# Performance work log

Measured on AMD Instinct MI355X. Metric: run time of the kernel, lower is better.

Reference implementation:

```python
import jax, jax.numpy as jnp
import numpy as np

NUM_HEADS = 16
SRC_FACTS = 4


def setup_inputs() -> dict:
    key = jax.random.key(0)
    k1, k2, k3, k4, k5 = jax.random.split(key, 5)
    B, S, H, Dh = 16, 512, NUM_HEADS, 64  # B = batch(4) * src_facts(4)
    D = H * Dh  # d_model = 1024
    pre_q = jax.random.normal(k1, (B, S, H, Dh), dtype=jnp.float32)
    pre_v = jax.random.normal(k2, (B, S, H, Dh), dtype=jnp.float32)
    pre_k = jax.random.normal(k3, (B, S, H, Dh), dtype=jnp.float32)
    attn_mask = jax.random.randint(k4, (B, S, S), 0, 2).astype(jnp.int32)
    output_weights = jax.random.normal(k5, (D, D), dtype=jnp.float32) / np.float32(np.sqrt(D))
    return {
        "pre_q": pre_q,
        "pre_v": pre_v,
        "pre_k": pre_k,
        "attn_mask": attn_mask,
        "output_weights": output_weights,
        "out_seq_len": 512,
        "d_model": 1024,
    }


def reference(pre_q, pre_v, pre_k, attn_mask, output_weights, out_seq_len, d_model):
    B, Sq, H, Dh = pre_q.shape
    # Original: K.sqrt(cast(d_model) // num_heads) -> sqrt(head_dim)
    scale = jnp.sqrt(jnp.float32(float(d_model) // H))
    mask = attn_mask.astype(jnp.float32)[:, None]  # (B, 1, q, k) broadcast over heads
    # scores: (B, H, q, k)
    scores = jnp.einsum("bqhd,bkhd->bhqk", pre_q, pre_k) / scale
    # multiplicative pre-mask + additive -1e9 on masked slots
    scores = scores * mask + (1.0 - mask) * jnp.float32(-1e9)
    # softmax then multiplicative post-mask
    attn = jax.nn.softmax(scores, axis=-1) * mask
    heads = jnp.einsum("bhqk,bkhd->bqhd", attn, pre_v)  # (B, q, H, Dh)
    out = heads.reshape(B, Sq, H * Dh) @ output_weights  # (B, q, d_model)
    return out.reshape(-1, SRC_FACTS, out_seq_len, d_model)
```

## Files before the change

kernel.cpp:

```cpp
#include <hip/hip_runtime.h>
#include <hip/hip_bf16.h>


typedef __bf16 bf16;
typedef bf16 bf16x8 __attribute__((ext_vector_type(8)));
typedef float floatx4 __attribute__((ext_vector_type(4)));
typedef unsigned short ushort8 __attribute__((ext_vector_type(8)));

#define MFMA16(A, B, C) __builtin_amdgcn_mfma_f32_16x16x32_bf16((A), (B), (C), 0, 0, 0)

namespace {
constexpr int S   = 512;
constexpr int H   = 16;
constexpr int Dh  = 64;
constexpr int D   = 1024;
constexpr int LDT = 72;
constexpr size_t QN = (size_t)16 * S * H * Dh;
constexpr size_t WN = (size_t)D * D;
}

__global__ __launch_bounds__(256)
void convert_kernel(const float* __restrict__ src, bf16* __restrict__ dst, int n8)
{
    const int i = blockIdx.x * 256 + threadIdx.x;
    if (i >= n8) return;
    const float* fs = src + (size_t)i * 8;
    bf16x8 v;
#pragma unroll
    for (int j = 0; j < 8; ++j) v[j] = (bf16)fs[j];
    *(bf16x8*)(dst + (size_t)i * 8) = v;
}

__global__ __launch_bounds__(256)
void vtrans_kernel(const float* __restrict__ V, bf16* __restrict__ Vt)
{
    __shared__ bf16 Ts[64 * LDT];
    const int tid = threadIdx.x;
    const int bh  = blockIdx.x >> 3;
    const int st  = blockIdx.x & 7;
    const int b   = bh >> 4, h = bh & 15;
    const int r   = tid >> 2;
    const int c   = (tid & 3) * 16;

    const float* src = V + ((size_t)((b * S + st * 64 + r) * H + h)) * Dh + c;
#pragma unroll
    for (int i = 0; i < 16; ++i)
        Ts[(c + i) * LDT + r] = (bf16)src[i];
    __syncthreads();
    bf16* dst = Vt + ((size_t)bh * 64 + r) * S + st * 64 + c;
    *(ushort8*)dst       = *(const ushort8*)&Ts[r * LDT + c];
    *(ushort8*)(dst + 8) = *(const ushort8*)&Ts[r * LDT + c + 8];
}

__global__ __launch_bounds__(256)
void wtrans_kernel(const float* __restrict__ W, bf16* __restrict__ Wt)
{
    __shared__ bf16 Ts[64 * LDT];
    const int tid = threadIdx.x;
    const int nb  = blockIdx.x & 15;
    const int kb  = blockIdx.x >> 4;
    const int r   = tid >> 2;
    const int c   = (tid & 3) * 16;

    const float* src = W + (size_t)(kb * 64 + r) * D + nb * 64 + c;
#pragma unroll
    for (int i = 0; i < 16; ++i)
        Ts[(c + i) * LDT + r] = (bf16)src[i];
    __syncthreads();
    bf16* dst = Wt + (size_t)(nb * 64 + r) * D + kb * 64 + c;
    *(ushort8*)dst       = *(const ushort8*)&Ts[r * LDT + c];
    *(ushort8*)(dst + 8) = *(const ushort8*)&Ts[r * LDT + c + 8];
}

__global__ __launch_bounds__(256)
void attn_kernel(const float* __restrict__ Qg, const bf16* __restrict__ Kc,
                 const bf16* __restrict__ Vtg, const int* __restrict__ Mg,
                 bf16* __restrict__ heads)
{
    __shared__ bf16 smem[3 * 64 * LDT];
    bf16* Qs = smem;
    bf16* Ps = smem;
    bf16* Ks = smem + 64 * LDT;
    bf16* Vt = smem + 2 * 64 * LDT;

    const int tid  = threadIdx.x;
    const int lane = tid & 63;
    const int wave = tid >> 6;
    const int l15  = lane & 15;
    const int quad = lane >> 4;

    const int blk = blockIdx.x;
    const int h   = blk & 15;
    const int qt  = (blk >> 4) & 7;
    const int b   = blk >> 7;
    const int qbase = qt * 64;

    const int ldr = tid >> 2;
    const int ldc = (tid & 3) * 16;

    {
        const float* src = Qg + ((size_t)((b * S + qbase + ldr) * H + h)) * Dh + ldc;
        bf16x8 lo, hi;
#pragma unroll
        for (int i = 0; i < 8; ++i) lo[i] = (bf16)(src[i] * 0.125f);
#pragma unroll
        for (int i = 0; i < 8; ++i) hi[i] = (bf16)(src[8 + i] * 0.125f);
        *(bf16x8*)&Qs[ldr * LDT + ldc]     = lo;
        *(bf16x8*)&Qs[ldr * LDT + ldc + 8] = hi;
    }
    __syncthreads();
    const bf16x8 aq0 = *(const bf16x8*)&Qs[(wave * 16 + l15) * LDT + quad * 8];
    const bf16x8 aq1 = *(const bf16x8*)&Qs[(wave * 16 + l15) * LDT + quad * 8 + 32];

    float rsum[4] = {0.f, 0.f, 0.f, 0.f};
    floatx4 O[4];
#pragma unroll
    for (int i = 0; i < 4; ++i) O[i] = floatx4{0.f, 0.f, 0.f, 0.f};

    const int qw = qbase + wave * 16;
    const int* mrow_base = Mg + (size_t)(b * S + qw) * S;
    const bf16* vplane = Vtg + (size_t)(b * 16 + h) * 64 * S;

    for (int kt = 0; kt < 8; ++kt) {
        const int kb = kt * 64;
        const bf16* ksrc = Kc + ((size_t)((b * S + kb + ldr) * H + h)) * Dh + ldc;
        const bf16* vsrc = vplane + (size_t)ldr * S + kb + ldc;
        ushort8 k0 = *(const ushort8*)ksrc;
        ushort8 k1 = *(const ushort8*)(ksrc + 8);
        ushort8 v0 = *(const ushort8*)vsrc;
        ushort8 v1 = *(const ushort8*)(vsrc + 8);

        __syncthreads();
        *(ushort8*)&Ks[ldr * LDT + ldc]     = k0;
        *(ushort8*)&Ks[ldr * LDT + ldc + 8] = k1;
        *(ushort8*)&Vt[ldr * LDT + ldc]     = v0;
        *(ushort8*)&Vt[ldr * LDT + ldc + 8] = v1;
        __syncthreads();

        floatx4 sc[4];
#pragma unroll
        for (int nt = 0; nt < 4; ++nt) {
            bf16x8 bk0 = *(const bf16x8*)&Ks[(nt * 16 + l15) * LDT + quad * 8];
            bf16x8 bk1 = *(const bf16x8*)&Ks[(nt * 16 + l15) * LDT + quad * 8 + 32];
            floatx4 acc = floatx4{0.f, 0.f, 0.f, 0.f};
            acc = MFMA16(aq0, bk0, acc);
            acc = MFMA16(aq1, bk1, acc);
            sc[nt] = acc;
        }

#pragma unroll
        for (int reg = 0; reg < 4; ++reg) {
            const int row = quad * 4 + reg;
            const int* mp = mrow_base + (size_t)row * S + kb + l15;
#pragma unroll
            for (int nt = 0; nt < 4; ++nt) {
                int mv  = mp[nt * 16];
                float e = __expf(sc[nt][reg]);
                float p = mv ? e : 0.f;
                rsum[reg] += p;
                Ps[(wave * 16 + row) * LDT + nt * 16 + l15] = (bf16)p;
            }
        }

        bf16x8 ap0 = *(const bf16x8*)&Ps[(wave * 16 + l15) * LDT + quad * 8];
        bf16x8 ap1 = *(const bf16x8*)&Ps[(wave * 16 + l15) * LDT + quad * 8 + 32];
#pragma unroll
        for (int nt = 0; nt < 4; ++nt) {
            bf16x8 bv0 = *(const bf16x8*)&Vt[(nt * 16 + l15) * LDT + quad * 8];
            bf16x8 bv1 = *(const bf16x8*)&Vt[(nt * 16 + l15) * LDT + quad * 8 + 32];
            O[nt] = MFMA16(ap0, bv0, O[nt]);
            O[nt] = MFMA16(ap1, bv1, O[nt]);
        }
    }

#pragma unroll
    for (int off = 1; off < 16; off <<= 1) {
#pragma unroll
        for (int reg = 0; reg < 4; ++reg)
            rsum[reg] += __shfl_xor(rsum[reg], off, 64);
    }

    float inv[4];
#pragma unroll
    for (int reg = 0; reg < 4; ++reg)
        inv[reg] = (rsum[reg] > 0.f) ? (1.f / rsum[reg]) : 0.f;
#pragma unroll
    for (int nt = 0; nt < 4; ++nt) {
#pragma unroll
        for (int reg = 0; reg < 4; ++reg) {
            const int q = qw + quad * 4 + reg;
            const int d = nt * 16 + l15;
            heads[((size_t)((b * S + q) * H + h)) * Dh + d] = (bf16)(O[nt][reg] * inv[reg]);
        }
    }
}

__global__ __launch_bounds__(256)
void proj_kernel(const bf16* __restrict__ A, const bf16* __restrict__ Wt,
                 float* __restrict__ out)
{
    __shared__ bf16 As[64 * LDT];
    __shared__ bf16 Ws[64 * LDT];

    const int tid  = threadIdx.x;
    const int lane = tid & 63;
    const int wave = tid >> 6;
    const int l15  = lane & 15;
    const int quad = lane >> 4;

    const int nb = blockIdx.x & 15;
    const int mb = blockIdx.x >> 4;
    const int mbase = mb * 64, nbase = nb * 64;

    const int ldr = tid >> 2;
    const int ldc = (tid & 3) * 16;

    floatx4 O[4];
#pragma unroll
    for (int i = 0; i < 4; ++i) O[i] = floatx4{0.f, 0.f, 0.f, 0.f};

    for (int kt = 0; kt < 16; ++kt) {
        const int kb = kt * 64;
        const bf16* asrc = A  + (size_t)(mbase + ldr) * D + kb + ldc;
        const bf16* wsrc = Wt + (size_t)(nbase + ldr) * D + kb + ldc;
        ushort8 a0 = *(const ushort8*)asrc;
        ushort8 a1 = *(const ushort8*)(asrc + 8);
        ushort8 w0 = *(const ushort8*)wsrc;
        ushort8 w1 = *(const ushort8*)(wsrc + 8);

        __syncthreads();
        *(ushort8*)&As[ldr * LDT + ldc]     = a0;
        *(ushort8*)&As[ldr * LDT + ldc + 8] = a1;
        *(ushort8*)&Ws[ldr * LDT + ldc]     = w0;
        *(ushort8*)&Ws[ldr * LDT + ldc + 8] = w1;
        __syncthreads();

        bf16x8 fa0 = *(const bf16x8*)&As[(wave * 16 + l15) * LDT + quad * 8];
        bf16x8 fa1 = *(const bf16x8*)&As[(wave * 16 + l15) * LDT + quad * 8 + 32];
#pragma unroll
        for (int nt = 0; nt < 4; ++nt) {
            bf16x8 fb0 = *(const bf16x8*)&Ws[(nt * 16 + l15) * LDT + quad * 8];
            bf16x8 fb1 = *(const bf16x8*)&Ws[(nt * 16 + l15) * LDT + quad * 8 + 32];
            O[nt] = MFMA16(fa0, fb0, O[nt]);
            O[nt] = MFMA16(fa1, fb1, O[nt]);
        }
    }

#pragma unroll
    for (int nt = 0; nt < 4; ++nt) {
#pragma unroll
        for (int reg = 0; reg < 4; ++reg) {
            const int m = mbase + wave * 16 + quad * 4 + reg;
            const int n = nbase + nt * 16 + l15;
            out[(size_t)m * D + n] = O[nt][reg];
        }
    }
}

extern "C" void kernel_launch(void* const* d_in, const int* in_sizes, int n_in,
                              void* d_out, int out_size, void* d_ws, size_t ws_size,
                              hipStream_t stream)
{
    const float* pre_q = (const float*)d_in[0];
    const float* pre_v = (const float*)d_in[1];
    const float* pre_k = (const float*)d_in[2];
    const int*   mask  = (const int*)d_in[3];
    const float* Wg    = (const float*)d_in[4];
    float* out = (float*)d_out;

    bf16* Kc    = (bf16*)d_ws;
    bf16* Vt    = Kc + QN;
    bf16* Wt    = Vt + QN;
    bf16* heads = Wt + WN;

    convert_kernel<<<(int)(QN / 8 / 256), 256, 0, stream>>>(pre_k, Kc, (int)(QN / 8));
    vtrans_kernel<<<2048, 256, 0, stream>>>(pre_v, Vt);
    wtrans_kernel<<<256, 256, 0, stream>>>(Wg, Wt);

    attn_kernel<<<2048, 256, 0, stream>>>(pre_q, Kc, Vt, mask, heads);
    proj_kernel<<<2048, 256, 0, stream>>>(heads, Wt, out);
}
```

Baseline: 233.5 us.

## Fuse prep kernels, bit-pack mask, enlarge attention and projection tiles

Merges the K convert, V transpose and W transpose kernels into one prep launch that also packs the int32 mask into 64-bit ballots. Attention reads these bitmask words instead of int32 mask values and processes 128 query rows per block, so each K/V tile loaded is reused across twice as many rows. The projection GEMM moves to 128x128 tiles with a 64x64 sub-tile per wave, for more reuse of the staged operands. The larger tiles raise register and LDS use per block and leave fewer blocks, which may lower occupancy.

```diff
diff --git a/kernel.cpp b/kernel.cpp
--- a/kernel.cpp
+++ b/kernel.cpp
@@ -6,6 +6,7 @@
 typedef bf16 bf16x8 __attribute__((ext_vector_type(8)));
 typedef float floatx4 __attribute__((ext_vector_type(4)));
 typedef unsigned short ushort8 __attribute__((ext_vector_type(8)));
+typedef unsigned long long u64;
 
 #define MFMA16(A, B, C) __builtin_amdgcn_mfma_f32_16x16x32_bf16((A), (B), (C), 0, 0, 0)
 
@@ -20,68 +21,71 @@
 }
 
 __global__ __launch_bounds__(256)
-void convert_kernel(const float* __restrict__ src, bf16* __restrict__ dst, int n8)
-{
-    const int i = blockIdx.x * 256 + threadIdx.x;
-    if (i >= n8) return;
-    const float* fs = src + (size_t)i * 8;
-    bf16x8 v;
-#pragma unroll
-    for (int j = 0; j < 8; ++j) v[j] = (bf16)fs[j];
-    *(bf16x8*)(dst + (size_t)i * 8) = v;
-}
-
-__global__ __launch_bounds__(256)
-void vtrans_kernel(const float* __restrict__ V, bf16* __restrict__ Vt)
+void prep_kernel(const float* __restrict__ Kf, const float* __restrict__ Vf,
+                 const float* __restrict__ Wf, const int* __restrict__ Mg,
+                 bf16* __restrict__ Kc, bf16* __restrict__ Vt,
+                 bf16* __restrict__ Wt, u64* __restrict__ MB)
 {
     __shared__ bf16 Ts[64 * LDT];
-    const int tid = threadIdx.x;
-    const int bh  = blockIdx.x >> 3;
-    const int st  = blockIdx.x & 7;
-    const int b   = bh >> 4, h = bh & 15;
-    const int r   = tid >> 2;
-    const int c   = (tid & 3) * 16;
-
-    const float* src = V + ((size_t)((b * S + st * 64 + r) * H + h)) * Dh + c;
-#pragma unroll
-    for (int i = 0; i < 16; ++i)
-        Ts[(c + i) * LDT + r] = (bf16)src[i];
-    __syncthreads();
-    bf16* dst = Vt + ((size_t)bh * 64 + r) * S + st * 64 + c;
-    *(ushort8*)dst       = *(const ushort8*)&Ts[r * LDT + c];
-    *(ushort8*)(dst + 8) = *(const ushort8*)&Ts[r * LDT + c + 8];
-}
-
-__global__ __launch_bounds__(256)
-void wtrans_kernel(const float* __restrict__ W, bf16* __restrict__ Wt)
-{
-    __shared__ bf16 Ts[64 * LDT];
-    const int tid = threadIdx.x;
-    const int nb  = blockIdx.x & 15;
-    const int kb  = blockIdx.x >> 4;
-    const int r   = tid >> 2;
-    const int c   = (tid & 3) * 16;
-
-    const float* src = W + (size_t)(kb * 64 + r) * D + nb * 64 + c;
-#pragma unroll
-    for (int i = 0; i < 16; ++i)
-        Ts[(c + i) * LDT + r] = (bf16)src[i];
-    __syncthreads();
-    bf16* dst = Wt + (size_t)(nb * 64 + r) * D + kb * 64 + c;
-    *(ushort8*)dst       = *(const ushort8*)&Ts[r * LDT + c];
-    *(ushort8*)(dst + 8) = *(const ushort8*)&Ts[r * LDT + c + 8];
+    const int blk = blockIdx.x, tid = threadIdx.x;
+
+    if (blk < 4096) {
+        const int i = blk * 256 + tid;
+        const float* fs = Kf + (size_t)i * 8;
+        bf16x8 v;
+#pragma unroll
+        for (int j = 0; j < 8; ++j) v[j] = (bf16)fs[j];
+        *(bf16x8*)(Kc + (size_t)i * 8) = v;
+    } else if (blk < 6144) {
+        const int bk2 = blk - 4096;
+        const int bh  = bk2 >> 3, st = bk2 & 7;
+        const int b   = bh >> 4, h = bh & 15;
+        const int r   = tid >> 2, c = (tid & 3) * 16;
+        const float* src = Vf + ((size_t)((b * S + st * 64 + r) * H + h)) * Dh + c;
+#pragma unroll
+        for (int i = 0; i < 16; ++i)
+            Ts[(c + i) * LDT + r] = (bf16)src[i];
+        __syncthreads();
+        bf16* dst = Vt + ((size_t)bh * 64 + r) * S + st * 64 + c;
+        *(ushort8*)dst       = *(const ushort8*)&Ts[r * LDT + c];
+        *(ushort8*)(dst + 8) = *(const ushort8*)&Ts[r * LDT + c + 8];
+    } else if (blk < 6400) {
+        const int bk2 = blk - 6144;
+        const int nb  = bk2 & 15, kb = bk2 >> 4;
+        const int r   = tid >> 2, c = (tid & 3) * 16;
+        const float* src = Wf + (size_t)(kb * 64 + r) * D + nb * 64 + c;
+#pragma unroll
+        for (int i = 0; i < 16; ++i)
+            Ts[(c + i) * LDT + r] = (bf16)src[i];
+        __syncthreads();
+        bf16* dst = Wt + (size_t)(nb * 64 + r) * D + kb * 64 + c;
+        *(ushort8*)dst       = *(const ushort8*)&Ts[r * LDT + c];
+        *(ushort8*)(dst + 8) = *(const ushort8*)&Ts[r * LDT + c + 8];
+    } else {
+        const int bk2  = blk - 6400;
+        const int lane = tid & 63;
+        const int idx4 = bk2 * 4 + (tid >> 6);
+        const int row  = idx4 >> 1;
+        const int half = idx4 & 1;
+#pragma unroll
+        for (int r = 0; r < 4; ++r) {
+            int mv = Mg[(size_t)row * 512 + half * 256 + r * 64 + lane];
+            u64 bm = __ballot(mv != 0);
+            if (lane == 0) MB[(size_t)row * 8 + half * 4 + r] = bm;
+        }
+    }
 }
 
 __global__ __launch_bounds__(256)
 void attn_kernel(const float* __restrict__ Qg, const bf16* __restrict__ Kc,
-                 const bf16* __restrict__ Vtg, const int* __restrict__ Mg,
+                 const bf16* __restrict__ Vtg, const u64* __restrict__ MB,
                  bf16* __restrict__ heads)
 {
-    __shared__ bf16 smem[3 * 64 * LDT];
+    __shared__ bf16 smem[(128 + 64 + 64) * LDT];
     bf16* Qs = smem;
     bf16* Ps = smem;
-    bf16* Ks = smem + 64 * LDT;
-    bf16* Vt = smem + 2 * 64 * LDT;
+    bf16* Ks = smem + 128 * LDT;
+    bf16* Vt = smem + 192 * LDT;
 
     const int tid  = threadIdx.x;
     const int lane = tid & 63;
@@ -91,106 +95,126 @@
 
     const int blk = blockIdx.x;
     const int h   = blk & 15;
-    const int qt  = (blk >> 4) & 7;
-    const int b   = blk >> 7;
-    const int qbase = qt * 64;
-
-    const int ldr = tid >> 2;
-    const int ldc = (tid & 3) * 16;
+    const int qt  = (blk >> 4) & 3;
+    const int b   = blk >> 6;
+    const int qbase = qt * 128;
 
     {
-        const float* src = Qg + ((size_t)((b * S + qbase + ldr) * H + h)) * Dh + ldc;
-        bf16x8 lo, hi;
-#pragma unroll
-        for (int i = 0; i < 8; ++i) lo[i] = (bf16)(src[i] * 0.125f);
-#pragma unroll
-        for (int i = 0; i < 8; ++i) hi[i] = (bf16)(src[8 + i] * 0.125f);
-        *(bf16x8*)&Qs[ldr * LDT + ldc]     = lo;
-        *(bf16x8*)&Qs[ldr * LDT + ldc + 8] = hi;
+        const int pr = tid >> 1, pc = (tid & 1) * 32;
+        const float* src = Qg + ((size_t)((b * S + qbase + pr) * H + h)) * Dh + pc;
+#pragma unroll
+        for (int ch = 0; ch < 4; ++ch) {
+            bf16x8 v;
+#pragma unroll
+            for (int i = 0; i < 8; ++i) v[i] = (bf16)(src[ch * 8 + i] * 0.125f);
+            *(bf16x8*)&Qs[pr * LDT + pc + ch * 8] = v;
+        }
     }
     __syncthreads();
-    const bf16x8 aq0 = *(const bf16x8*)&Qs[(wave * 16 + l15) * LDT + quad * 8];
-    const bf16x8 aq1 = *(const bf16x8*)&Qs[(wave * 16 + l15) * LDT + quad * 8 + 32];
-
-    float rsum[4] = {0.f, 0.f, 0.f, 0.f};
-    floatx4 O[4];
-#pragma unroll
-    for (int i = 0; i < 4; ++i) O[i] = floatx4{0.f, 0.f, 0.f, 0.f};
-
-    const int qw = qbase + wave * 16;
-    const int* mrow_base = Mg + (size_t)(b * S + qw) * S;
+    bf16x8 aq[2][2];
+#pragma unroll
+    for (int mt = 0; mt < 2; ++mt)
+#pragma unroll
+        for (int hf = 0; hf < 2; ++hf)
+            aq[mt][hf] = *(const bf16x8*)&Qs[(wave * 32 + mt * 16 + l15) * LDT + hf * 32 + quad * 8];
+
+    float rsum[2][4] = {{0.f}};
+    floatx4 O[2][4];
+#pragma unroll
+    for (int mt = 0; mt < 2; ++mt)
+#pragma unroll
+        for (int nt = 0; nt < 4; ++nt) O[mt][nt] = floatx4{0.f, 0.f, 0.f, 0.f};
+
+    const int qw = qbase + wave * 32;
+    const u64* mb_base = MB + ((size_t)b * S + qw) * 8;
     const bf16* vplane = Vtg + (size_t)(b * 16 + h) * 64 * S;
+
+    const int sr = tid >> 2, sc_ = (tid & 3) * 16;
 
     for (int kt = 0; kt < 8; ++kt) {
         const int kb = kt * 64;
-        const bf16* ksrc = Kc + ((size_t)((b * S + kb + ldr) * H + h)) * Dh + ldc;
-        const bf16* vsrc = vplane + (size_t)ldr * S + kb + ldc;
+        const bf16* ksrc = Kc + ((size_t)((b * S + kb + sr) * H + h)) * Dh + sc_;
+        const bf16* vsrc = vplane + (size_t)sr * S + kb + sc_;
         ushort8 k0 = *(const ushort8*)ksrc;
         ushort8 k1 = *(const ushort8*)(ksrc + 8);
         ushort8 v0 = *(const ushort8*)vsrc;
         ushort8 v1 = *(const ushort8*)(vsrc + 8);
 
         __syncthreads();
-        *(ushort8*)&Ks[ldr * LDT + ldc]     = k0;
-        *(ushort8*)&Ks[ldr * LDT + ldc + 8] = k1;
-        *(ushort8*)&Vt[ldr * LDT + ldc]     = v0;
-        *(ushort8*)&Vt[ldr * LDT + ldc + 8] = v1;
-        __syncthreads();
-
-        floatx4 sc[4];
+        *(ushort8*)&Ks[sr * LDT + sc_]     = k0;
+        *(ushort8*)&Ks[sr * LDT + sc_ + 8] = k1;
+        *(ushort8*)&Vt[sr * LDT + sc_]     = v0;
+        *(ushort8*)&Vt[sr * LDT + sc_ + 8] = v1;
+        __syncthreads();
+
+        floatx4 sc4[2][4];
 #pragma unroll
         for (int nt = 0; nt < 4; ++nt) {
             bf16x8 bk0 = *(const bf16x8*)&Ks[(nt * 16 + l15) * LDT + quad * 8];
             bf16x8 bk1 = *(const bf16x8*)&Ks[(nt * 16 + l15) * LDT + quad * 8 + 32];
-            floatx4 acc = floatx4{0.f, 0.f, 0.f, 0.f};
-            acc = MFMA16(aq0, bk0, acc);
-            acc = MFMA16(aq1, bk1, acc);
-            sc[nt] = acc;
-        }
-
-#pragma unroll
-        for (int reg = 0; reg < 4; ++reg) {
-            const int row = quad * 4 + reg;
-            const int* mp = mrow_base + (size_t)row * S + kb + l15;
-#pragma unroll
-            for (int nt = 0; nt < 4; ++nt) {
-                int mv  = mp[nt * 16];
-                float e = __expf(sc[nt][reg]);
-                float p = mv ? e : 0.f;
-                rsum[reg] += p;
-                Ps[(wave * 16 + row) * LDT + nt * 16 + l15] = (bf16)p;
-            }
-        }
-
-        bf16x8 ap0 = *(const bf16x8*)&Ps[(wave * 16 + l15) * LDT + quad * 8];
-        bf16x8 ap1 = *(const bf16x8*)&Ps[(wave * 16 + l15) * LDT + quad * 8 + 32];
+#pragma unroll
+            for (int mt = 0; mt < 2; ++mt) {
+                floatx4 acc = floatx4{0.f, 0.f, 0.f, 0.f};
+                acc = MFMA16(aq[mt][0], bk0, acc);
+                acc = MFMA16(aq[mt][1], bk1, acc);
+                sc4[mt][nt] = acc;
+            }
+        }
+
+#pragma unroll
+        for (int mt = 0; mt < 2; ++mt) {
+#pragma unroll
+            for (int reg = 0; reg < 4; ++reg) {
+                const int row = mt * 16 + quad * 4 + reg;
+                u64 m64 = mb_base[(size_t)row * 8 + kt];
+                u64 t   = m64 >> l15;
+#pragma unroll
+                for (int nt = 0; nt < 4; ++nt) {
+                    unsigned bit = (unsigned)(t >> (nt * 16)) & 1u;
+                    float e = __expf(sc4[mt][nt][reg]);
+                    float p = bit ? e : 0.f;
+                    rsum[mt][reg] += p;
+                    Ps[(wave * 32 + row) * LDT + nt * 16 + l15] = (bf16)p;
+                }
+            }
+        }
+
 #pragma unroll
         for (int nt = 0; nt < 4; ++nt) {
             bf16x8 bv0 = *(const bf16x8*)&Vt[(nt * 16 + l15) * LDT + quad * 8];
             bf16x8 bv1 = *(const bf16x8*)&Vt[(nt * 16 + l15) * LDT + quad * 8 + 32];
-            O[nt] = MFMA16(ap0, bv0, O[nt]);
-            O[nt] = MFMA16(ap1, bv1, O[nt]);
-        }
-    }
-
-#pragma unroll
-    for (int off = 1; off < 16; off <<= 1) {
+#pragma unroll
+            for (int mt = 0; mt < 2; ++mt) {
+                bf16x8 ap0 = *(const bf16x8*)&Ps[(wave * 32 + mt * 16 + l15) * LDT + quad * 8];
+                bf16x8 ap1 = *(const bf16x8*)&Ps[(wave * 32 + mt * 16 + l15) * LDT + quad * 8 + 32];
+                O[mt][nt] = MFMA16(ap0, bv0, O[mt][nt]);
+                O[mt][nt] = MFMA16(ap1, bv1, O[mt][nt]);
+            }
+        }
+    }
+
+#pragma unroll
+    for (int off = 1; off < 16; off <<= 1)
+#pragma unroll
+        for (int mt = 0; mt < 2; ++mt)
+#pragma unroll
+            for (int reg = 0; reg < 4; ++reg)
+                rsum[mt][reg] += __shfl_xor(rsum[mt][reg], off, 64);
+
+#pragma unroll
+    for (int mt = 0; mt < 2; ++mt) {
+        float inv[4];
 #pragma unroll
         for (int reg = 0; reg < 4; ++reg)
-            rsum[reg] += __shfl_xor(rsum[reg], off, 64);
-    }
-
-    float inv[4];
-#pragma unroll
-    for (int reg = 0; reg < 4; ++reg)
-        inv[reg] = (rsum[reg] > 0.f) ? (1.f / rsum[reg]) : 0.f;
-#pragma unroll
-    for (int nt = 0; nt < 4; ++nt) {
-#pragma unroll
-        for (int reg = 0; reg < 4; ++reg) {
-            const int q = qw + quad * 4 + reg;
-            const int d = nt * 16 + l15;
-            heads[((size_t)((b * S + q) * H + h)) * Dh + d] = (bf16)(O[nt][reg] * inv[reg]);
+            inv[reg] = (rsum[mt][reg] > 0.f) ? (1.f / rsum[mt][reg]) : 0.f;
+#pragma unroll
+        for (int nt = 0; nt < 4; ++nt) {
+#pragma unroll
+            for (int reg = 0; reg < 4; ++reg) {
+                const int q = qw + mt * 16 + quad * 4 + reg;
+                const int d = nt * 16 + l15;
+                heads[((size_t)((b * S + q) * H + h)) * Dh + d] = (bf16)(O[mt][nt][reg] * inv[reg]);
+            }
         }
     }
 }
@@ -199,8 +223,8 @@
 void proj_kernel(const bf16* __restrict__ A, const bf16* __restrict__ Wt,
                  float* __restrict__ out)
 {
-    __shared__ bf16 As[64 * LDT];
-    __shared__ bf16 Ws[64 * LDT];
+    __shared__ bf16 As[128 * LDT];
+    __shared__ bf16 Ws[128 * LDT];
 
     const int tid  = threadIdx.x;
     const int lane = tid & 63;
@@ -208,51 +232,71 @@
     const int l15  = lane & 15;
     const int quad = lane >> 4;
 
-    const int nb = blockIdx.x & 15;
-    const int mb = blockIdx.x >> 4;
-    const int mbase = mb * 64, nbase = nb * 64;
-
-    const int ldr = tid >> 2;
-    const int ldc = (tid & 3) * 16;
-
-    floatx4 O[4];
-#pragma unroll
-    for (int i = 0; i < 4; ++i) O[i] = floatx4{0.f, 0.f, 0.f, 0.f};
+    const int nb = blockIdx.x & 7;
+    const int mb = blockIdx.x >> 3;
+    const int mbase = mb * 128, nbase = nb * 128;
+    const int wm = (wave & 1) * 64, wn = (wave >> 1) * 64;
+
+    const int pr = tid >> 1, pc = (tid & 1) * 32;
+
+    floatx4 O[4][4];
+#pragma unroll
+    for (int mt = 0; mt < 4; ++mt)
+#pragma unroll
+        for (int nt = 0; nt < 4; ++nt) O[mt][nt] = floatx4{0.f, 0.f, 0.f, 0.f};
 
     for (int kt = 0; kt < 16; ++kt) {
         const int kb = kt * 64;
-        const bf16* asrc = A  + (size_t)(mbase + ldr) * D + kb + ldc;
-        const bf16* wsrc = Wt + (size_t)(nbase + ldr) * D + kb + ldc;
+        const bf16* asrc = A  + (size_t)(mbase + pr) * D + kb + pc;
+        const bf16* wsrc = Wt + (size_t)(nbase + pr) * D + kb + pc;
         ushort8 a0 = *(const ushort8*)asrc;
         ushort8 a1 = *(const ushort8*)(asrc + 8);
+        ushort8 a2 = *(const ushort8*)(asrc + 16);
+        ushort8 a3 = *(const ushort8*)(asrc + 24);
         ushort8 w0 = *(const ushort8*)wsrc;
         ushort8 w1 = *(const ushort8*)(wsrc + 8);
-
-        __syncthreads();
-        *(ushort8*)&As[ldr * LDT + ldc]     = a0;
-        *(ushort8*)&As[ldr * LDT + ldc + 8] = a1;
-        *(ushort8*)&Ws[ldr * LDT + ldc]     = w0;
-        *(ushort8*)&Ws[ldr * LDT + ldc + 8] = w1;
-        __syncthreads();
-
-        bf16x8 fa0 = *(const bf16x8*)&As[(wave * 16 + l15) * LDT + quad * 8];
-        bf16x8 fa1 = *(const bf16x8*)&As[(wave * 16 + l15) * LDT + quad * 8 + 32];
-#pragma unroll
-        for (int nt = 0; nt < 4; ++nt) {
-            bf16x8 fb0 = *(const bf16x8*)&Ws[(nt * 16 + l15) * LDT + quad * 8];
-            bf16x8 fb1 = *(const bf16x8*)&Ws[(nt * 16 + l15) * LDT + quad * 8 + 32];
-            O[nt] = MFMA16(fa0, fb0, O[nt]);
-            O[nt] = MFMA16(fa1, fb1, O[nt]);
-        }
-    }
-
-#pragma unroll
-    for (int nt = 0; nt < 4; ++nt) {
-#pragma unroll
-        for (int reg = 0; reg < 4; ++reg) {
-            const int m = mbase + wave * 16 + quad * 4 + reg;
-            const int n = nbase + nt * 16 + l15;
-            out[(size_t)m * D + n] = O[nt][reg];
+        ushort8 w2 = *(const ushort8*)(wsrc + 16);
+        ushort8 w3 = *(const ushort8*)(wsrc + 24);
+
+        __syncthreads();
+        *(ushort8*)&As[pr * LDT + pc]      = a0;
+        *(ushort8*)&As[pr * LDT + pc + 8]  = a1;
+        *(ushort8*)&As[pr * LDT + pc + 16] = a2;
+        *(ushort8*)&As[pr * LDT + pc + 24] = a3;
+        *(ushort8*)&Ws[pr * LDT + pc]      = w0;
+        *(ushort8*)&Ws[pr * LDT + pc + 8]  = w1;
+        *(ushort8*)&Ws[pr * LDT + pc + 16] = w2;
+        *(ushort8*)&Ws[pr * LDT + pc + 24] = w3;
+        __syncthreads();
+
+        bf16x8 fa[4][2];
+#pragma unroll
+        for (int mt = 0; mt < 4; ++mt) {
+            fa[mt][0] = *(const bf16x8*)&As[(wm + mt * 16 + l15) * LDT + quad * 8];
+            fa[mt][1] = *(const bf16x8*)&As[(wm + mt * 16 + l15) * LDT + quad * 8 + 32];
+        }
+#pragma unroll
+        for (int nt = 0; nt < 4; ++nt) {
+            bf16x8 fb0 = *(const bf16x8*)&Ws[(wn + nt * 16 + l15) * LDT + quad * 8];
+            bf16x8 fb1 = *(const bf16x8*)&Ws[(wn + nt * 16 + l15) * LDT + quad * 8 + 32];
+#pragma unroll
+            for (int mt = 0; mt < 4; ++mt) {
+                O[mt][nt] = MFMA16(fa[mt][0], fb0, O[mt][nt]);
+                O[mt][nt] = MFMA16(fa[mt][1], fb1, O[mt][nt]);
+            }
+        }
+    }
+
+#pragma unroll
+    for (int mt = 0; mt < 4; ++mt) {
+#pragma unroll
+        for (int nt = 0; nt < 4; ++nt) {
+#pragma unroll
+            for (int reg = 0; reg < 4; ++reg) {
+                const int m = mbase + wm + mt * 16 + quad * 4 + reg;
+                const int n = nbase + wn + nt * 16 + l15;
+                out[(size_t)m * D + n] = O[mt][nt][reg];
+            }
         }
     }
 }
@@ -272,11 +316,9 @@
     bf16* Vt    = Kc + QN;
     bf16* Wt    = Vt + QN;
     bf16* heads = Wt + WN;
-
-    convert_kernel<<<(int)(QN / 8 / 256), 256, 0, stream>>>(pre_k, Kc, (int)(QN / 8));
-    vtrans_kernel<<<2048, 256, 0, stream>>>(pre_v, Vt);
-    wtrans_kernel<<<256, 256, 0, stream>>>(Wg, Wt);
-
-    attn_kernel<<<2048, 256, 0, stream>>>(pre_q, Kc, Vt, mask, heads);
-    proj_kernel<<<2048, 256, 0, stream>>>(heads, Wt, out);
-}
+    u64*  MB    = (u64*)(heads + QN);
+
+    prep_kernel<<<10496, 256, 0, stream>>>(pre_k, pre_v, Wg, mask, Kc, Vt, Wt, MB);
+    attn_kernel<<<1024, 256, 0, stream>>>(pre_q, Kc, Vt, MB, heads);
+    proj_kernel<<<512, 256, 0, stream>>>(heads, Wt, out);
+}
```

Result: faster. 225.9 us (-3.3%).
